# Kernel optimization log

Measured on AMD Instinct MI355X. Metric: run time of the kernel, lower is better.

The kernel has to match this reference:

```python
import jax, jax.numpy as jnp
import numpy as np

N_NODES = 20000
N_EDGES = 320000
IN_CH = 256
HID_CH = 512


def setup_inputs() -> dict:
    key = jax.random.key(0)
    k_x, k_e, k_w1, k_w2 = jax.random.split(key, 4)
    x = jax.random.normal(k_x, (N_NODES, IN_CH), dtype=jnp.float32)
    edge_index = jax.random.randint(k_e, (2, N_EDGES), 0, N_NODES, dtype=jnp.int32)
    # Glorot-style init for the two GCNConv weight matrices; PyG GCNConv bias init is zeros.
    W1 = jax.random.normal(k_w1, (IN_CH, HID_CH), dtype=jnp.float32) * (1.0 / np.sqrt(IN_CH))
    b1 = jnp.zeros((HID_CH,), dtype=jnp.float32)
    W2 = jax.random.normal(k_w2, (HID_CH, HID_CH), dtype=jnp.float32) * (1.0 / np.sqrt(HID_CH))
    b2 = jnp.zeros((HID_CH,), dtype=jnp.float32)
    return {"x": x, "edge_index": edge_index, "W1": W1, "b1": b1, "W2": W2, "b2": b2}


def _gcn_conv(x, W, b, src, dst, n_nodes):
    """PyG GCNConv: linear transform, then sym-normalized aggregation with self-loops."""
    h = x @ W  # [N, H]
    # in-degree on dst, +1 for the implicit self-loop
    deg = jnp.zeros((n_nodes,), dtype=h.dtype).at[dst].add(1.0) + 1.0
    dinv = jax.lax.rsqrt(deg)  # deg >= 1 always
    norm = dinv[src] * dinv[dst]  # [E]
    msg = h[src] * norm[:, None]  # [E, H] gathered, normalized messages
    agg = jax.ops.segment_sum(msg, dst, num_segments=n_nodes)  # scatter-add to targets
    # self-loop contribution: norm for edge i->i is dinv[i]^2
    return agg + h * (dinv * dinv)[:, None] + b


def reference(x, edge_index, W1, b1, W2, b2):
    src, dst = edge_index[0], edge_index[1]
    n = x.shape[0]
    h = jax.nn.relu(_gcn_conv(x, W1, b1, src, dst, n))
    # dropout(p=0.2) is identity in eval mode
    return _gcn_conv(h, W2, b2, src, dst, n)
```

## Files before the change

kernel.cpp:

```cpp
#include <hip/hip_runtime.h>

#define N_NODES 20000
#define N_EDGES 320000
#define IN_CH 256
#define HID_CH 512
#define NB_SCAN ((N_NODES + 255) / 256)

typedef unsigned short u16;
typedef __attribute__((ext_vector_type(4))) float f32x4;
typedef __attribute__((ext_vector_type(8))) short bf16x8;
typedef __attribute__((ext_vector_type(4))) u16 u16x4;
typedef __attribute__((ext_vector_type(8))) u16 u16x8;

__device__ __forceinline__ float bf2f(u16 h) { return __uint_as_float((unsigned)h << 16); }
__device__ __forceinline__ u16 f2bf(float f) {
    unsigned u = __float_as_uint(f);
    return (u16)((u + 0x7fffu + ((u >> 16) & 1u)) >> 16);
}

__global__ void zero2_kernel(int* __restrict__ a, int* __restrict__ b, int n) {
    int i = blockIdx.x * blockDim.x + threadIdx.x;
    if (i < n) { a[i] = 0; b[i] = 0; }
}

__global__ void count_deg_kernel(const int* __restrict__ dst, int* __restrict__ deg, int E) {
    int i = blockIdx.x * blockDim.x + threadIdx.x;
    if (i < E) atomicAdd(&deg[dst[i]], 1);
}

__global__ __launch_bounds__(256) void scan_pass1(const int* __restrict__ deg,
                                                  float* __restrict__ dinv,
                                                  int* __restrict__ bsum, int N) {
    __shared__ int tmp[256];
    int t = threadIdx.x;
    int i = blockIdx.x * 256 + t;
    int d = (i < N) ? deg[i] : 0;
    if (i < N) dinv[i] = rsqrtf((float)d + 1.0f);
    tmp[t] = d;
    __syncthreads();
#pragma unroll
    for (int off = 128; off > 0; off >>= 1) {
        if (t < off) tmp[t] += tmp[t + off];
        __syncthreads();
    }
    if (t == 0) bsum[blockIdx.x] = tmp[0];
}

__global__ __launch_bounds__(128) void scan_pass2(int* __restrict__ bsum, int NB) {
    __shared__ int tmp[128];
    int t = threadIdx.x;
    tmp[t] = (t < NB) ? bsum[t] : 0;
    __syncthreads();
#pragma unroll
    for (int off = 1; off < 128; off <<= 1) {
        int v = (t >= off) ? tmp[t - off] : 0;
        __syncthreads();
        tmp[t] += v;
        __syncthreads();
    }
    if (t < NB) bsum[t] = (t == 0) ? 0 : tmp[t - 1];
}

__global__ __launch_bounds__(256) void scan_pass3(const int* __restrict__ deg,
                                                  const int* __restrict__ bsum,
                                                  int* __restrict__ row_ptr, int N, int E) {
    __shared__ int tmp[256];
    int t = threadIdx.x;
    int i = blockIdx.x * 256 + t;
    int d = (i < N) ? deg[i] : 0;
    tmp[t] = d;
    __syncthreads();
#pragma unroll
    for (int off = 1; off < 256; off <<= 1) {
        int v = (t >= off) ? tmp[t - off] : 0;
        __syncthreads();
        tmp[t] += v;
        __syncthreads();
    }
    if (i < N) row_ptr[i] = bsum[blockIdx.x] + tmp[t] - d;
    if (i == 0) row_ptr[N] = E;
}

__global__ void scatter_edges_kernel(const int* __restrict__ src, const int* __restrict__ dst,
                                     const int* __restrict__ row_ptr, int* __restrict__ cursor,
                                     const float* __restrict__ dinv, int2* __restrict__ epair,
                                     int E) {
    int e = blockIdx.x * blockDim.x + threadIdx.x;
    if (e >= E) return;
    int d = dst[e];
    int s = src[e];
    int pos = row_ptr[d] + atomicAdd(&cursor[d], 1);
    epair[pos] = make_int2(s, __float_as_int(dinv[s]));
}

__global__ void f32_to_bf16_kernel(const float* __restrict__ in, u16* __restrict__ out, int n4) {
    int i = blockIdx.x * blockDim.x + threadIdx.x;
    if (i >= n4) return;
    float4 v = ((const float4*)in)[i];
    u16x4 o = {f2bf(v.x), f2bf(v.y), f2bf(v.z), f2bf(v.w)};
    ((u16x4*)out)[i] = o;
}

__global__ __launch_bounds__(256) void convert_w_kernel(const float* __restrict__ W1,
                                                        u16* __restrict__ hi1, u16* __restrict__ lo1,
                                                        const float* __restrict__ W2,
                                                        u16* __restrict__ hi2, u16* __restrict__ lo2) {
    __shared__ float t[64][65];
    int b = blockIdx.x;
    const float* W;
    u16 *hi, *lo;
    int K;
    if (b < 32) { W = W1; hi = hi1; lo = lo1; K = IN_CH; }
    else        { b -= 32; W = W2; hi = hi2; lo = lo2; K = HID_CH; }
    const int N = HID_CH;
    int k0 = (b >> 3) * 64, n0 = (b & 7) * 64;
    int c = threadIdx.x & 63, r4 = threadIdx.x >> 6;
#pragma unroll
    for (int i = 0; i < 16; ++i) {
        int r = i * 4 + r4;
        t[r][c] = W[(size_t)(k0 + r) * N + n0 + c];
    }
    __syncthreads();
#pragma unroll
    for (int i = 0; i < 16; ++i) {
        int n = i * 4 + r4;
        float f = t[c][n];
        u16 hb = f2bf(f);
        size_t o = (size_t)(n0 + n) * K + k0 + c;
        hi[o] = hb;
        lo[o] = f2bf(f - bf2f(hb));
    }
}

template <int C, int SLICES>
__global__ __launch_bounds__(256) void gather_agg_kernel(
        const u16* __restrict__ h, const int2* __restrict__ epair,
        const int* __restrict__ row_ptr, const float* __restrict__ dinv,
        u16* __restrict__ z, int N) {
    int bid = blockIdx.x;
    int nb, s;
    if (SLICES == 8) {
        nb = bid >> 3;
        s = bid & 7;
    } else {
        nb = (bid >> 3) * 2 + (bid & 1);
        s = (bid & 7) >> 1;
    }
    int t = threadIdx.x;
    int grp = t >> 3;
    int u = t & 7;
    int n = nb * 32 + grp;
    bool alive = (n < N);
    int nn = alive ? n : (N - 1);
    float dn = dinv[nn];
    const u16* hbase = h + s * 64 + u * 8;
    float acc[8];
    {
        u16x8 ws = *(const u16x8*)(hbase + (size_t)nn * C);
        float sf = dn * dn;
#pragma unroll
        for (int j = 0; j < 8; ++j) acc[j] = bf2f(ws[j]) * sf;
    }
    int e0 = row_ptr[nn];
    int e1 = alive ? row_ptr[nn + 1] : e0;
    int e = e0;
    for (; e + 4 <= e1; e += 4) {
        int2 p0 = epair[e + 0], p1 = epair[e + 1], p2 = epair[e + 2], p3 = epair[e + 3];
        u16x8 w0 = *(const u16x8*)(hbase + (size_t)p0.x * C);
        u16x8 w1 = *(const u16x8*)(hbase + (size_t)p1.x * C);
        u16x8 w2 = *(const u16x8*)(hbase + (size_t)p2.x * C);
        u16x8 w3 = *(const u16x8*)(hbase + (size_t)p3.x * C);
        float n0 = __int_as_float(p0.y) * dn, n1 = __int_as_float(p1.y) * dn;
        float n2 = __int_as_float(p2.y) * dn, n3 = __int_as_float(p3.y) * dn;
#pragma unroll
        for (int j = 0; j < 8; ++j) {
            acc[j] = fmaf(bf2f(w0[j]), n0, acc[j]);
            acc[j] = fmaf(bf2f(w1[j]), n1, acc[j]);
            acc[j] = fmaf(bf2f(w2[j]), n2, acc[j]);
            acc[j] = fmaf(bf2f(w3[j]), n3, acc[j]);
        }
    }
    for (; e < e1; ++e) {
        int2 p = epair[e];
        u16x8 w = *(const u16x8*)(hbase + (size_t)p.x * C);
        float nr = __int_as_float(p.y) * dn;
#pragma unroll
        for (int j = 0; j < 8; ++j) acc[j] = fmaf(bf2f(w[j]), nr, acc[j]);
    }
    if (alive) {
        u16x8 vh;
#pragma unroll
        for (int j = 0; j < 8; ++j) vh[j] = f2bf(acc[j]);
        *(u16x8*)(z + (size_t)n * C + s * 64 + u * 8) = vh;
    }
}

template <int K, bool RELU, bool OUT_BF16>
__global__ __launch_bounds__(512, 4) void gemm_mfma_kernel(
        const u16* __restrict__ A, const u16* __restrict__ Bh, const u16* __restrict__ Bl,
        const float* __restrict__ bias, void* __restrict__ Cout, int M, int N) {
    __shared__ u16 lds[3][12288];
    const int tid = threadIdx.x;
    const int lane = tid & 63;
    const int wid = tid >> 6;

    const int nmt = (M + 127) / 128;
    const int total = nmt * 4;
    int bid = blockIdx.x;
    int q = total >> 3, r = total & 7;
    int xcd = bid & 7, pp = bid >> 3;
    int lin = (xcd < r) ? (xcd * (q + 1) + pp) : (r * (q + 1) + (xcd - r) * q + pp);
    const int bm = (lin >> 2) * 128;
    const int bn = (lin & 3) * 128;

    const int wm = (wid & 1) * 64;
    const int wn = (wid >> 1) * 32;

    f32x4 acc[4][2];
#pragma unroll
    for (int i = 0; i < 4; ++i)
#pragma unroll
        for (int j = 0; j < 2; ++j) acc[i][j] = (f32x4){0.f, 0.f, 0.f, 0.f};

    const int srow = (wid << 4) + (lane >> 2);
    const int scb = (((lane & 3) ^ ((lane >> 3) & 3)) << 4);
    const char* srcA  = (const char*)(A  + (size_t)min(bm + srow, M - 1) * K) + scb;
    const char* srcBh = (const char*)(Bh + (size_t)(bn + srow) * K) + scb;
    const char* srcBl = (const char*)(Bl + (size_t)(bn + srow) * K) + scb;
    const int dstoff = wid << 10;

#define GLL(srcp, dstb)                                                                  \
    __builtin_amdgcn_global_load_lds(                                                    \
        (const __attribute__((address_space(1))) void*)(srcp),                           \
        (__attribute__((address_space(3))) void*)((char*)&lds[buf][0] + (dstb)), 16, 0, 0)

#define STAGE(bufv, k0)                                                                  \
    do {                                                                                 \
        int buf = (bufv);                                                                \
        size_t kb2 = (size_t)(k0) * 2;                                                   \
        GLL(srcA + kb2, dstoff);                                                         \
        GLL(srcBh + kb2, 8192 + dstoff);                                                 \
        GLL(srcBl + kb2, 16384 + dstoff);                                                \
    } while (0)

    STAGE(0, 0);
    STAGE(1, 32);

    const int NT = K / 32;
    const int kb = (lane >> 4) << 4;
#pragma unroll
    for (int t = 0; t < NT; ++t) {
        if (t + 1 < NT) {
            asm volatile("s_waitcnt vmcnt(3)" ::: "memory");
        } else {
            asm volatile("s_waitcnt vmcnt(0)" ::: "memory");
        }
        __builtin_amdgcn_s_barrier();
        asm volatile("" ::: "memory");

        if (t + 2 < NT) STAGE((t + 2) % 3, (t + 2) * 32);

        const char* L = (const char*)&lds[t % 3][0];
        bf16x8 a[4], b_h[2], b_l[2];
#pragma unroll
        for (int i = 0; i < 4; ++i) {
            int ra = wm + i * 16 + (lane & 15);
            int off = ra * 64 + (kb ^ (((ra >> 1) & 3) << 4));
            a[i] = *(const bf16x8*)(L + off);
        }
#pragma unroll
        for (int j = 0; j < 2; ++j) {
            int rb = wn + j * 16 + (lane & 15);
            int off = rb * 64 + (kb ^ (((rb >> 1) & 3) << 4));
            b_h[j] = *(const bf16x8*)(L + 8192 + off);
            b_l[j] = *(const bf16x8*)(L + 16384 + off);
        }
#pragma unroll
        for (int i = 0; i < 4; ++i)
#pragma unroll
            for (int j = 0; j < 2; ++j) {
                acc[i][j] = __builtin_amdgcn_mfma_f32_16x16x32_bf16(a[i], b_h[j], acc[i][j], 0, 0, 0);
                acc[i][j] = __builtin_amdgcn_mfma_f32_16x16x32_bf16(a[i], b_l[j], acc[i][j], 0, 0, 0);
            }
    }
#undef STAGE
#undef GLL

#pragma unroll
    for (int j = 0; j < 2; ++j) {
        int gc = bn + wn + j * 16 + (lane & 15);
        float bv = bias[gc];
#pragma unroll
        for (int i = 0; i < 4; ++i) {
#pragma unroll
            for (int t = 0; t < 4; ++t) {
                int gr = bm + wm + i * 16 + ((lane >> 4) << 2) + t;
                if (gr < M) {
                    float v = acc[i][j][t] + bv;
                    if (RELU) v = fmaxf(v, 0.f);
                    if (OUT_BF16)
                        ((u16*)Cout)[(size_t)gr * N + gc] = f2bf(v);
                    else
                        ((float*)Cout)[(size_t)gr * N + gc] = v;
                }
            }
        }
    }
}

extern "C" void kernel_launch(void* const* d_in, const int* in_sizes, int n_in,
                              void* d_out, int out_size, void* d_ws, size_t ws_size,
                              hipStream_t stream) {
    const float* x  = (const float*)d_in[0];
    const int*   ei = (const int*)d_in[1];
    const float* W1 = (const float*)d_in[2];
    const float* b1 = (const float*)d_in[3];
    const float* W2 = (const float*)d_in[4];
    const float* b2 = (const float*)d_in[5];
    const int* src = ei;
    const int* dst = ei + N_EDGES;

    char* ws = (char*)d_ws;
    size_t off = 0;
    auto alloc = [&](size_t bytes) {
        void* p = ws + off;
        off = (off + bytes + 255) & ~(size_t)255;
        return p;
    };
    int*   deg     = (int*)alloc(N_NODES * 4);
    int*   cursor  = (int*)alloc(N_NODES * 4);
    int*   row_ptr = (int*)alloc((N_NODES + 1) * 4);
    float* dinv    = (float*)alloc(N_NODES * 4);
    int*   bsum    = (int*)alloc(NB_SCAN * 4);
    int2*  epair   = (int2*)alloc((size_t)N_EDGES * 8);
    u16*   wt1_hi  = (u16*)alloc((size_t)IN_CH * HID_CH * 2);
    u16*   wt1_lo  = (u16*)alloc((size_t)IN_CH * HID_CH * 2);
    u16*   wt2_hi  = (u16*)alloc((size_t)HID_CH * HID_CH * 2);
    u16*   wt2_lo  = (u16*)alloc((size_t)HID_CH * HID_CH * 2);
    u16*   xb      = (u16*)alloc((size_t)N_NODES * IN_CH * 2);
    u16*   z1      = (u16*)alloc((size_t)N_NODES * IN_CH * 2);
    u16*   z2      = (u16*)alloc((size_t)N_NODES * HID_CH * 2);
    u16*   h1      = (u16*)d_out;

    zero2_kernel<<<NB_SCAN, 256, 0, stream>>>(deg, cursor, N_NODES);
    count_deg_kernel<<<(N_EDGES + 255) / 256, 256, 0, stream>>>(dst, deg, N_EDGES);
    scan_pass1<<<NB_SCAN, 256, 0, stream>>>(deg, dinv, bsum, N_NODES);
    scan_pass2<<<1, 128, 0, stream>>>(bsum, NB_SCAN);
    scan_pass3<<<NB_SCAN, 256, 0, stream>>>(deg, bsum, row_ptr, N_NODES, N_EDGES);
    scatter_edges_kernel<<<(N_EDGES + 255) / 256, 256, 0, stream>>>(src, dst, row_ptr, cursor,
                                                                    dinv, epair, N_EDGES);

    f32_to_bf16_kernel<<<(N_NODES * IN_CH / 4 + 255) / 256, 256, 0, stream>>>(
        x, xb, N_NODES * IN_CH / 4);
    convert_w_kernel<<<96, 256, 0, stream>>>(W1, wt1_hi, wt1_lo, W2, wt2_hi, wt2_lo);

    const int NMT = (N_NODES + 127) / 128;
    const int NB32 = (N_NODES + 31) / 32;
    gather_agg_kernel<IN_CH, 4><<<((NB32 + 1) / 2) * 8, 256, 0, stream>>>(
        xb, epair, row_ptr, dinv, z1, N_NODES);
    gemm_mfma_kernel<IN_CH, true, true><<<NMT * 4, 512, 0, stream>>>(
        z1, wt1_hi, wt1_lo, b1, h1, N_NODES, HID_CH);

    gather_agg_kernel<HID_CH, 8><<<NB32 * 8, 256, 0, stream>>>(
        h1, epair, row_ptr, dinv, z2, N_NODES);
    gemm_mfma_kernel<HID_CH, false, false><<<NMT * 4, 512, 0, stream>>>(
        z2, wt2_hi, wt2_lo, b2, (float*)d_out, N_NODES, HID_CH);
}
```

Baseline: 164.3 us.

## Load low-half B fragments directly to registers and deepen LDS pipeline to four stages

```diff
diff --git a/kernel.cpp b/kernel.cpp
--- a/kernel.cpp
+++ b/kernel.cpp
@@ -199,7 +199,7 @@
 __global__ __launch_bounds__(512, 4) void gemm_mfma_kernel(
         const u16* __restrict__ A, const u16* __restrict__ Bh, const u16* __restrict__ Bl,
         const float* __restrict__ bias, void* __restrict__ Cout, int M, int N) {
-    __shared__ u16 lds[3][12288];
+    __shared__ u16 lds[4][8192];
     const int tid = threadIdx.x;
     const int lane = tid & 63;
     const int wid = tid >> 6;
@@ -226,8 +226,12 @@
     const int scb = (((lane & 3) ^ ((lane >> 3) & 3)) << 4);
     const char* srcA  = (const char*)(A  + (size_t)min(bm + srow, M - 1) * K) + scb;
     const char* srcBh = (const char*)(Bh + (size_t)(bn + srow) * K) + scb;
-    const char* srcBl = (const char*)(Bl + (size_t)(bn + srow) * K) + scb;
     const int dstoff = wid << 10;
+
+    const int kfrag = (lane >> 4) << 3;
+    const u16* Bl0p = Bl + (size_t)(bn + wn + (lane & 15)) * K + kfrag;
+    const u16* Bl1p = Bl + (size_t)(bn + wn + 16 + (lane & 15)) * K + kfrag;
+    bf16x8 blr[2][2];
 
 #define GLL(srcp, dstb)                                                                  \
     __builtin_amdgcn_global_load_lds(                                                    \
@@ -240,28 +244,47 @@
         size_t kb2 = (size_t)(k0) * 2;                                                   \
         GLL(srcA + kb2, dstoff);                                                         \
         GLL(srcBh + kb2, 8192 + dstoff);                                                 \
-        GLL(srcBl + kb2, 16384 + dstoff);                                                \
     } while (0)
 
+#define BLLOAD(setv, k0)                                                                 \
+    do {                                                                                 \
+        int set = (setv);                                                                \
+        blr[set][0] = *(const bf16x8*)(Bl0p + (k0));                                     \
+        blr[set][1] = *(const bf16x8*)(Bl1p + (k0));                                     \
+    } while (0)
+
     STAGE(0, 0);
+    __builtin_amdgcn_sched_barrier(0);
     STAGE(1, 32);
+    __builtin_amdgcn_sched_barrier(0);
+    STAGE(2, 64);
+    __builtin_amdgcn_sched_barrier(0);
+    BLLOAD(0, 0);
+    __builtin_amdgcn_sched_barrier(0);
 
     const int NT = K / 32;
     const int kb = (lane >> 4) << 4;
 #pragma unroll
     for (int t = 0; t < NT; ++t) {
-        if (t + 1 < NT) {
-            asm volatile("s_waitcnt vmcnt(3)" ::: "memory");
+        if (t == 0) {
+            asm volatile("s_waitcnt vmcnt(6)" ::: "memory");
+        } else if (t == NT - 1) {
+            asm volatile("s_waitcnt vmcnt(4)" ::: "memory");
+        } else if (t == 1 || t == NT - 2) {
+            asm volatile("s_waitcnt vmcnt(6)" ::: "memory");
         } else {
-            asm volatile("s_waitcnt vmcnt(0)" ::: "memory");
+            asm volatile("s_waitcnt vmcnt(8)" ::: "memory");
         }
         __builtin_amdgcn_s_barrier();
         asm volatile("" ::: "memory");
 
-        if (t + 2 < NT) STAGE((t + 2) % 3, (t + 2) * 32);
-
-        const char* L = (const char*)&lds[t % 3][0];
-        bf16x8 a[4], b_h[2], b_l[2];
+        if (t + 3 < NT) STAGE((t + 3) & 3, (t + 3) * 32);
+        __builtin_amdgcn_sched_barrier(0);
+        if (t + 1 < NT) BLLOAD((t + 1) & 1, (t + 1) * 32);
+        __builtin_amdgcn_sched_barrier(0);
+
+        const char* L = (const char*)&lds[t & 3][0];
+        bf16x8 a[4], b_h[2];
 #pragma unroll
         for (int i = 0; i < 4; ++i) {
             int ra = wm + i * 16 + (lane & 15);
@@ -273,18 +296,18 @@
             int rb = wn + j * 16 + (lane & 15);
             int off = rb * 64 + (kb ^ (((rb >> 1) & 3) << 4));
             b_h[j] = *(const bf16x8*)(L + 8192 + off);
-            b_l[j] = *(const bf16x8*)(L + 16384 + off);
         }
 #pragma unroll
         for (int i = 0; i < 4; ++i)
 #pragma unroll
             for (int j = 0; j < 2; ++j) {
                 acc[i][j] = __builtin_amdgcn_mfma_f32_16x16x32_bf16(a[i], b_h[j], acc[i][j], 0, 0, 0);
-                acc[i][j] = __builtin_amdgcn_mfma_f32_16x16x32_bf16(a[i], b_l[j], acc[i][j], 0, 0, 0);
+                acc[i][j] = __builtin_amdgcn_mfma_f32_16x16x32_bf16(a[i], blr[t & 1][j], acc[i][j], 0, 0, 0);
             }
     }
 #undef STAGE
 #undef GLL
+#undef BLLOAD
 
 #pragma unroll
     for (int j = 0; j < 2; ++j) {
```

Measured after the change: 181.6 us. +10.5%, slower.
